# Kernel optimization log

Hardware: AMD Instinct MI355X
Metric: run time of the kernel (lower is better)

The kernel has to match this reference:

```python
import jax, jax.numpy as jnp
import numpy as np

T, B, C = 1024, 8, 256
H, F = 8, 512
D = C // H  # head dim = 32
EPS = 1e-5


def _layernorm(x, g, b):
    mu = jnp.mean(x, axis=-1, keepdims=True)
    var = jnp.var(x, axis=-1, keepdims=True)
    return (x - mu) * jax.lax.rsqrt(var + EPS) * g + b


def setup_inputs() -> dict:
    key = jax.random.key(0)
    ks = jax.random.split(key, 12)
    s = 0.02
    return {
        "x_TBC": jax.random.normal(ks[0], (T, B, C), jnp.float32),
        "key_padding_mask": jnp.zeros((B, T), dtype=bool),
        "edge_bias": jax.random.normal(ks[1], (B, H, T, T), jnp.float32),
        "ln1_g": jnp.ones((C,), jnp.float32),
        "ln1_b": jnp.zeros((C,), jnp.float32),
        "ln2_g": jnp.ones((C,), jnp.float32),
        "ln2_b": jnp.zeros((C,), jnp.float32),
        "w_qkv": jax.random.normal(ks[2], (3 * C, C), jnp.float32) * s,
        "b_qkv": jnp.zeros((3 * C,), jnp.float32),
        "w_o": jax.random.normal(ks[3], (C, C), jnp.float32) * s,
        "b_o": jnp.zeros((C,), jnp.float32),
        "w1": jax.random.normal(ks[4], (F, C), jnp.float32) * s,
        "b1": jnp.zeros((F,), jnp.float32),
        "w2": jax.random.normal(ks[5], (C, F), jnp.float32) * s,
        "b2": jnp.zeros((C,), jnp.float32),
    }


def _attn(y, key_padding_mask, edge_bias, w_qkv, b_qkv, w_o, b_o):
    # y: [T,B,C]
    qkv = jnp.einsum('tbc,ec->tbe', y, w_qkv) + b_qkv  # [T,B,3C]
    q, k, v = jnp.split(qkv, 3, axis=-1)
    def heads(z):  # [T,B,C] -> [B,H,T,D]
        return z.reshape(T, B, H, D).transpose(1, 2, 0, 3)
    q, k, v = heads(q), heads(k), heads(v)
    scale = 1.0 / jnp.sqrt(jnp.asarray(D, jnp.float32))
    scores = jnp.einsum('bhqd,bhkd->bhqk', q * scale, k) + edge_bias
    neg = jnp.asarray(-1e9, scores.dtype)
    scores = jnp.where(key_padding_mask[:, None, None, :], neg, scores)
    probs = jax.nn.softmax(scores, axis=-1)
    o = jnp.einsum('bhqk,bhkd->bhqd', probs, v)  # [B,H,T,D]
    o = o.transpose(2, 0, 1, 3).reshape(T, B, C)
    return jnp.einsum('tbc,ec->tbe', o, w_o) + b_o


def reference(x_TBC, key_padding_mask, edge_bias, ln1_g, ln1_b, ln2_g, ln2_b,
              w_qkv, b_qkv, w_o, b_o, w1, b1, w2, b2):
    # pre-LN: LN -> attn(edge bias) -> residual, LN -> FFN -> residual
    y = _layernorm(x_TBC, ln1_g, ln1_b)
    y = _attn(y, key_padding_mask, edge_bias, w_qkv, b_qkv, w_o, b_o)
    x = x_TBC + y
    y = _layernorm(x, ln2_g, ln2_b)
    y = jax.nn.gelu(jnp.einsum('tbc,fc->tbf', y, w1) + b1, approximate=False)
    y = jnp.einsum('tbf,cf->tbc', y, w2) + b2
    return x + y
```

## Files before the change

### kernel.cpp

```cpp
#include <hip/hip_runtime.h>
#include <hip/hip_bf16.h>
#include <cmath>

#define T_DIM 1024
#define B_DIM 8
#define C_DIM 256
#define H_DIM 8
#define D_DIM 32
#define F_DIM 512

typedef __attribute__((ext_vector_type(4))) float f32x4;
typedef __attribute__((ext_vector_type(8))) short bf16x8;

static __device__ __forceinline__ unsigned short f2bf(float f) {
    union { float f; unsigned u; } v; v.f = f;
    unsigned r = v.u + 0x7fff + ((v.u >> 16) & 1);
    return (unsigned short)(r >> 16);
}

__global__ __launch_bounds__(256) void convert_weights(const float* __restrict__ wqkv,
                                                       const float* __restrict__ wo,
                                                       const float* __restrict__ w1,
                                                       const float* __restrict__ w2,
                                                       unsigned short* __restrict__ dst)
{
    int e = blockIdx.x * 256 + threadIdx.x;
    const float* src; int off;
    if (e < 196608)      { src = wqkv; off = 0; }
    else if (e < 262144) { src = wo;   off = 196608; }
    else if (e < 393216) { src = w1;   off = 262144; }
    else                 { src = w2;   off = 393216; }
    dst[e] = f2bf(src[e - off]);
}

__global__ __launch_bounds__(256) void ln_bf16(const float* __restrict__ x,
                                               const float* __restrict__ g,
                                               const float* __restrict__ bta,
                                               unsigned short* __restrict__ y)
{
    int row  = blockIdx.x * 4 + (threadIdx.x >> 6);
    int lane = threadIdx.x & 63;
    float4 v = ((const float4*)(x + (size_t)row * C_DIM))[lane];
    float s  = v.x + v.y + v.z + v.w;
    float ss = v.x * v.x + v.y * v.y + v.z * v.z + v.w * v.w;
#pragma unroll
    for (int off = 1; off < 64; off <<= 1) {
        s  += __shfl_xor(s, off);
        ss += __shfl_xor(ss, off);
    }
    float mu   = s * (1.0f / C_DIM);
    float var  = ss * (1.0f / C_DIM) - mu * mu;
    float rstd = rsqrtf(var + 1e-5f);
    float4 gv = ((const float4*)g)[lane];
    float4 bv = ((const float4*)bta)[lane];
    ushort4 o;
    o.x = f2bf((v.x - mu) * rstd * gv.x + bv.x);
    o.y = f2bf((v.y - mu) * rstd * gv.y + bv.y);
    o.z = f2bf((v.z - mu) * rstd * gv.z + bv.z);
    o.w = f2bf((v.w - mu) * rstd * gv.w + bv.w);
    ((ushort4*)(y + (size_t)row * C_DIM))[lane] = o;
}

template<int EPI>
__global__ __launch_bounds__(256) void gemm_mfma(const unsigned short* __restrict__ A,
                                                 const unsigned short* __restrict__ W,
                                                 const float* __restrict__ bias,
                                                 const float* __restrict__ R,
                                                 void* __restrict__ outv,
                                                 int N, int K)
{
    __shared__ unsigned short A_s[128][40];
    __shared__ unsigned short W_s[64][40];
    int tid  = threadIdx.x;
    int lane = tid & 63;
    int wv   = tid >> 6;
    int l15  = lane & 15, lg = lane >> 4;
    int row0 = blockIdx.y * 128;
    int col0 = blockIdx.x * 64;

    f32x4 acc[2][4] = {};
    for (int k0 = 0; k0 < K; k0 += 32) {
#pragma unroll
        for (int i = 0; i < 8; i++) {
            int p = tid + i * 256;
            int m = p >> 4, dp = (p & 15) * 2;
            *(uint32_t*)&A_s[m][dp] = *(const uint32_t*)(A + (size_t)(row0 + m) * K + k0 + dp);
        }
#pragma unroll
        for (int i = 0; i < 4; i++) {
            int p = tid + i * 256;
            int n = p >> 4, dp = (p & 15) * 2;
            *(uint32_t*)&W_s[n][dp] = *(const uint32_t*)(W + (size_t)(col0 + n) * K + k0 + dp);
        }
        __syncthreads();
        bf16x8 af[2], wf[4];
#pragma unroll
        for (int mb = 0; mb < 2; mb++)
            af[mb] = *(const bf16x8*)&A_s[wv * 32 + mb * 16 + l15][lg * 8];
#pragma unroll
        for (int nb = 0; nb < 4; nb++)
            wf[nb] = *(const bf16x8*)&W_s[nb * 16 + l15][lg * 8];
#pragma unroll
        for (int mb = 0; mb < 2; mb++)
#pragma unroll
            for (int nb = 0; nb < 4; nb++)
                acc[mb][nb] = __builtin_amdgcn_mfma_f32_16x16x32_bf16(af[mb], wf[nb], acc[mb][nb], 0, 0, 0);
        __syncthreads();
    }
#pragma unroll
    for (int nb = 0; nb < 4; nb++) {
        int c = col0 + nb * 16 + l15;
        float bv = bias[c];
#pragma unroll
        for (int mb = 0; mb < 2; mb++) {
#pragma unroll
            for (int r = 0; r < 4; r++) {
                int rowm = row0 + wv * 32 + mb * 16 + lg * 4 + r;
                float v = acc[mb][nb][r] + bv;
                if (EPI == 1) v = 0.5f * v * (1.0f + erff(v * 0.70710678118654752f));
                if (EPI == 2) {
                    v += R[(size_t)rowm * N + c];
                    ((float*)outv)[(size_t)rowm * N + c] = v;
                } else {
                    ((unsigned short*)outv)[(size_t)rowm * N + c] = f2bf(v);
                }
            }
        }
    }
}

__global__ __launch_bounds__(256) void attn_mfma(const unsigned short* __restrict__ qkv,
                                                 const float* __restrict__ bias,
                                                 const unsigned char* __restrict__ mask,
                                                 unsigned short* __restrict__ o)
{
    __shared__ unsigned short K_s[64][40];
    __shared__ unsigned short Vt_s[32][72];
    __shared__ unsigned short P_s[4][16][72];
    __shared__ float bias_s[64][68];
    __shared__ unsigned char m_s[64];

    int tid  = threadIdx.x;
    int lane = tid & 63;
    int wv   = tid >> 6;
    int l15  = lane & 15, lg = lane >> 4;
    int bh = blockIdx.y, b = bh >> 3, hh = bh & 7;
    int q0 = blockIdx.x * 64;
    int qw = q0 + wv * 16;
    const float scale = 0.17677669529663687f;

    bf16x8 qf = *(const bf16x8*)(qkv + ((size_t)(qw + l15) * B_DIM + b) * 768 + hh * 32 + lg * 8);

    float m_run = -INFINITY, l_run = 0.0f;
    f32x4 oacc[2] = {};

    for (int k0 = 0; k0 < T_DIM; k0 += 64) {
#pragma unroll
        for (int i = 0; i < 4; i++) {
            int p = tid + i * 256;
            int kv = p >> 4, dp = (p & 15) * 2;
            const unsigned short* src = qkv + ((size_t)(k0 + kv) * B_DIM + b) * 768 + hh * 32;
            uint32_t kk = *(const uint32_t*)(src + 256 + dp);
            uint32_t vv = *(const uint32_t*)(src + 512 + dp);
            *(uint32_t*)&K_s[kv][dp] = kk;
            Vt_s[dp][kv]     = (unsigned short)(vv & 0xffff);
            Vt_s[dp + 1][kv] = (unsigned short)(vv >> 16);
        }
#pragma unroll
        for (int i = 0; i < 4; i++) {
            int p = tid + i * 256;
            int q = p >> 4, c4 = (p & 15) * 4;
            *(f32x4*)&bias_s[q][c4] =
                *(const f32x4*)(bias + ((size_t)bh * T_DIM + q0 + q) * T_DIM + k0 + c4);
        }
        if (tid < 64) m_s[tid] = mask[b * T_DIM + k0 + tid];
        __syncthreads();

        float sv[4][4];
        float tmax = -INFINITY;
#pragma unroll
        for (int kb = 0; kb < 4; kb++) {
            bf16x8 kf = *(const bf16x8*)&K_s[kb * 16 + l15][lg * 8];
            f32x4 z = {0.0f, 0.0f, 0.0f, 0.0f};
            f32x4 sc = __builtin_amdgcn_mfma_f32_16x16x32_bf16(kf, qf, z, 0, 0, 0);
            f32x4 bv = *(const f32x4*)&bias_s[wv * 16 + l15][kb * 16 + lg * 4];
            uint32_t mw = *(const uint32_t*)&m_s[kb * 16 + lg * 4];
#pragma unroll
            for (int r = 0; r < 4; r++) {
                float s = sc[r] * scale + bv[r];
                if ((mw >> (8 * r)) & 0xff) s = -1e9f;
                sv[kb][r] = s;
                tmax = fmaxf(tmax, s);
            }
        }
        tmax = fmaxf(tmax, __shfl_xor(tmax, 16));
        tmax = fmaxf(tmax, __shfl_xor(tmax, 32));
        float m_new = fmaxf(m_run, tmax);
        float corr = __expf(m_run - m_new);
        m_run = m_new;

        float ls = 0.0f;
#pragma unroll
        for (int kb = 0; kb < 4; kb++) {
            float p0 = __expf(sv[kb][0] - m_new);
            float p1 = __expf(sv[kb][1] - m_new);
            float p2 = __expf(sv[kb][2] - m_new);
            float p3 = __expf(sv[kb][3] - m_new);
            ls += (p0 + p1) + (p2 + p3);
            uint2 pw;
            pw.x = (uint32_t)f2bf(p0) | ((uint32_t)f2bf(p1) << 16);
            pw.y = (uint32_t)f2bf(p2) | ((uint32_t)f2bf(p3) << 16);
            *(uint2*)&P_s[wv][l15][kb * 16 + lg * 4] = pw;
        }
        ls += __shfl_xor(ls, 16);
        ls += __shfl_xor(ls, 32);
        l_run = l_run * corr + ls;
#pragma unroll
        for (int db = 0; db < 2; db++)
#pragma unroll
            for (int r = 0; r < 4; r++) oacc[db][r] *= corr;

#pragma unroll
        for (int h = 0; h < 2; h++) {
            bf16x8 pf = *(const bf16x8*)&P_s[wv][l15][h * 32 + lg * 8];
#pragma unroll
            for (int db = 0; db < 2; db++) {
                bf16x8 vf = *(const bf16x8*)&Vt_s[db * 16 + l15][h * 32 + lg * 8];
                oacc[db] = __builtin_amdgcn_mfma_f32_16x16x32_bf16(vf, pf, oacc[db], 0, 0, 0);
            }
        }
        __syncthreads();
    }

    float inv = 1.0f / l_run;
#pragma unroll
    for (int db = 0; db < 2; db++)
#pragma unroll
        for (int r = 0; r < 4; r++)
            bias_s[wv * 16 + l15][db * 16 + lg * 4 + r] = oacc[db][r] * inv;
    __syncthreads();
#pragma unroll
    for (int i = 0; i < 8; i++) {
        int p = tid + i * 256;
        int lq = p >> 5, d = p & 31;
        o[((size_t)(q0 + lq) * B_DIM + b) * C_DIM + hh * 32 + d] = f2bf(bias_s[lq][d]);
    }
}

extern "C" void kernel_launch(void* const* d_in, const int* in_sizes, int n_in,
                              void* d_out, int out_size, void* d_ws, size_t ws_size,
                              hipStream_t stream)
{
    const float* x            = (const float*)d_in[0];
    const unsigned char* mask = (const unsigned char*)d_in[1];
    const float* bias         = (const float*)d_in[2];
    const float* ln1g         = (const float*)d_in[3];
    const float* ln1b         = (const float*)d_in[4];
    const float* ln2g         = (const float*)d_in[5];
    const float* ln2b         = (const float*)d_in[6];
    const float* wqkv         = (const float*)d_in[7];
    const float* bqkv         = (const float*)d_in[8];
    const float* wo           = (const float*)d_in[9];
    const float* bo           = (const float*)d_in[10];
    const float* w1           = (const float*)d_in[11];
    const float* b1           = (const float*)d_in[12];
    const float* w2           = (const float*)d_in[13];
    const float* b2           = (const float*)d_in[14];
    float* out = (float*)d_out;
    char* ws   = (char*)d_ws;

    unsigned short* wbf     = (unsigned short*)ws;
    unsigned short* wqkv_bf = wbf;
    unsigned short* wo_bf   = wbf + 196608;
    unsigned short* w1_bf   = wbf + 262144;
    unsigned short* w2_bf   = wbf + 393216;
    unsigned short* y_bf    = (unsigned short*)(ws + (1u << 20));
    unsigned short* qkv_bf  = (unsigned short*)(ws + 5u * (1u << 20));
    unsigned short* o_bf    = (unsigned short*)(ws + 17u * (1u << 20));
    float*          x1      = (float*)(ws + 21u * (1u << 20));
    unsigned short* h_bf    = (unsigned short*)(ws + 29u * (1u << 20));

    const int M = T_DIM * B_DIM;

    convert_weights<<<2048, 256, 0, stream>>>(wqkv, wo, w1, w2, wbf);
    ln_bf16<<<M / 4, 256, 0, stream>>>(x, ln1g, ln1b, y_bf);
    gemm_mfma<0><<<dim3(768 / 64, M / 128), 256, 0, stream>>>(y_bf, wqkv_bf, bqkv, nullptr, qkv_bf, 768, 256);
    attn_mfma<<<dim3(T_DIM / 64, B_DIM * H_DIM), 256, 0, stream>>>(qkv_bf, bias, mask, o_bf);
    gemm_mfma<2><<<dim3(256 / 64, M / 128), 256, 0, stream>>>(o_bf, wo_bf, bo, x, x1, 256, 256);
    ln_bf16<<<M / 4, 256, 0, stream>>>(x1, ln2g, ln2b, y_bf);
    gemm_mfma<1><<<dim3(512 / 64, M / 128), 256, 0, stream>>>(y_bf, w1_bf, b1, nullptr, h_bf, 512, 256);
    gemm_mfma<2><<<dim3(256 / 64, M / 128), 256, 0, stream>>>(h_bf, w2_bf, b2, x1, out, 256, 512);
}
```

Measured before the change: 139.4 us.

## Use direct global-to-LDS loads with XOR swizzle and register-resident attention bias

The GEMM now stages A and W tiles with global_load_lds 16-byte transfers into XOR-swizzled shared memory and uses a larger K step of 64 per barrier. The attention kernel loads K tiles the same way, reads the edge bias straight into registers issued before the barrier instead of staging it through LDS, and writes output directly from registers. This aims to cut VGPR round-trips, bank conflicts and barrier count in the memory-bound bias stream, at the cost of relying on swizzle index math being correct and more live registers.

```diff
diff --git a/kernel.cpp b/kernel.cpp
--- a/kernel.cpp
+++ b/kernel.cpp
@@ -16,6 +16,13 @@
     union { float f; unsigned u; } v; v.f = f;
     unsigned r = v.u + 0x7fff + ((v.u >> 16) & 1);
     return (unsigned short)(r >> 16);
+}
+
+static __device__ __forceinline__ void gload_lds16(const void* g, void* l) {
+    __builtin_amdgcn_global_load_lds(
+        (const __attribute__((address_space(1))) unsigned int*)g,
+        (__attribute__((address_space(3))) unsigned int*)l,
+        16, 0, 0);
 }
 
 __global__ __launch_bounds__(256) void convert_weights(const float* __restrict__ wqkv,
@@ -69,8 +76,8 @@
                                                  void* __restrict__ outv,
                                                  int N, int K)
 {
-    __shared__ unsigned short A_s[128][40];
-    __shared__ unsigned short W_s[64][40];
+    __shared__ __align__(16) unsigned short A_s[128 * 64];
+    __shared__ __align__(16) unsigned short W_s[64 * 64];
     int tid  = threadIdx.x;
     int lane = tid & 63;
     int wv   = tid >> 6;
@@ -79,32 +86,41 @@
     int col0 = blockIdx.x * 64;
 
     f32x4 acc[2][4] = {};
-    for (int k0 = 0; k0 < K; k0 += 32) {
-#pragma unroll
-        for (int i = 0; i < 8; i++) {
-            int p = tid + i * 256;
-            int m = p >> 4, dp = (p & 15) * 2;
-            *(uint32_t*)&A_s[m][dp] = *(const uint32_t*)(A + (size_t)(row0 + m) * K + k0 + dp);
-        }
+    for (int k0 = 0; k0 < K; k0 += 64) {
 #pragma unroll
         for (int i = 0; i < 4; i++) {
-            int p = tid + i * 256;
-            int n = p >> 4, dp = (p & 15) * 2;
-            *(uint32_t*)&W_s[n][dp] = *(const uint32_t*)(W + (size_t)(col0 + n) * K + k0 + dp);
+            int u = (wv * 4 + i) * 64 + lane;
+            int r = u >> 3, c = u & 7;
+            gload_lds16(A + (size_t)(row0 + r) * K + k0 + ((c ^ (r & 7)) * 8),
+                        &A_s[(size_t)(wv * 4 + i) * 512]);
+        }
+#pragma unroll
+        for (int j = 0; j < 2; j++) {
+            int u = (wv * 2 + j) * 64 + lane;
+            int r = u >> 3, c = u & 7;
+            gload_lds16(W + (size_t)(col0 + r) * K + k0 + ((c ^ (r & 7)) * 8),
+                        &W_s[(size_t)(wv * 2 + j) * 512]);
         }
         __syncthreads();
-        bf16x8 af[2], wf[4];
-#pragma unroll
-        for (int mb = 0; mb < 2; mb++)
-            af[mb] = *(const bf16x8*)&A_s[wv * 32 + mb * 16 + l15][lg * 8];
-#pragma unroll
-        for (int nb = 0; nb < 4; nb++)
-            wf[nb] = *(const bf16x8*)&W_s[nb * 16 + l15][lg * 8];
-#pragma unroll
-        for (int mb = 0; mb < 2; mb++)
-#pragma unroll
-            for (int nb = 0; nb < 4; nb++)
-                acc[mb][nb] = __builtin_amdgcn_mfma_f32_16x16x32_bf16(af[mb], wf[nb], acc[mb][nb], 0, 0, 0);
+#pragma unroll
+        for (int kk = 0; kk < 2; kk++) {
+            bf16x8 af[2], wf[4];
+#pragma unroll
+            for (int mb = 0; mb < 2; mb++) {
+                int rowa = wv * 32 + mb * 16 + l15;
+                af[mb] = *(const bf16x8*)&A_s[rowa * 64 + (((kk * 4 + lg) ^ (l15 & 7)) * 8)];
+            }
+#pragma unroll
+            for (int nb = 0; nb < 4; nb++) {
+                int roww = nb * 16 + l15;
+                wf[nb] = *(const bf16x8*)&W_s[roww * 64 + (((kk * 4 + lg) ^ (l15 & 7)) * 8)];
+            }
+#pragma unroll
+            for (int mb = 0; mb < 2; mb++)
+#pragma unroll
+                for (int nb = 0; nb < 4; nb++)
+                    acc[mb][nb] = __builtin_amdgcn_mfma_f32_16x16x32_bf16(af[mb], wf[nb], acc[mb][nb], 0, 0, 0);
+        }
         __syncthreads();
     }
 #pragma unroll
@@ -134,10 +150,9 @@
                                                  const unsigned char* __restrict__ mask,
                                                  unsigned short* __restrict__ o)
 {
-    __shared__ unsigned short K_s[64][40];
+    __shared__ __align__(16) unsigned short K_s[64 * 32];
     __shared__ unsigned short Vt_s[32][72];
     __shared__ unsigned short P_s[4][16][72];
-    __shared__ float bias_s[64][68];
     __shared__ unsigned char m_s[64];
 
     int tid  = threadIdx.x;
@@ -151,43 +166,46 @@
 
     bf16x8 qf = *(const bf16x8*)(qkv + ((size_t)(qw + l15) * B_DIM + b) * 768 + hh * 32 + lg * 8);
 
+    int krow = wv * 16 + (lane >> 2);
+    int kc   = lane & 3;
+    int kswz = (kc ^ (krow & 3)) * 8;
+    const unsigned short* kfp = &K_s[l15 * 32 + ((lg ^ (l15 & 3)) * 8)];
+
+    const float* bptr = bias + ((size_t)bh * T_DIM + q0 + wv * 16 + l15) * T_DIM + lg * 4;
+
     float m_run = -INFINITY, l_run = 0.0f;
     f32x4 oacc[2] = {};
 
     for (int k0 = 0; k0 < T_DIM; k0 += 64) {
+        f32x4 bb0 = *(const f32x4*)(bptr + k0);
+        f32x4 bb1 = *(const f32x4*)(bptr + k0 + 16);
+        f32x4 bb2 = *(const f32x4*)(bptr + k0 + 32);
+        f32x4 bb3 = *(const f32x4*)(bptr + k0 + 48);
+        gload_lds16(qkv + ((size_t)(k0 + krow) * B_DIM + b) * 768 + 256 + hh * 32 + kswz,
+                    &K_s[(size_t)wv * 512]);
 #pragma unroll
         for (int i = 0; i < 4; i++) {
             int p = tid + i * 256;
             int kv = p >> 4, dp = (p & 15) * 2;
-            const unsigned short* src = qkv + ((size_t)(k0 + kv) * B_DIM + b) * 768 + hh * 32;
-            uint32_t kk = *(const uint32_t*)(src + 256 + dp);
-            uint32_t vv = *(const uint32_t*)(src + 512 + dp);
-            *(uint32_t*)&K_s[kv][dp] = kk;
+            uint32_t vv = *(const uint32_t*)(qkv + ((size_t)(k0 + kv) * B_DIM + b) * 768 + 512 + hh * 32 + dp);
             Vt_s[dp][kv]     = (unsigned short)(vv & 0xffff);
             Vt_s[dp + 1][kv] = (unsigned short)(vv >> 16);
         }
-#pragma unroll
-        for (int i = 0; i < 4; i++) {
-            int p = tid + i * 256;
-            int q = p >> 4, c4 = (p & 15) * 4;
-            *(f32x4*)&bias_s[q][c4] =
-                *(const f32x4*)(bias + ((size_t)bh * T_DIM + q0 + q) * T_DIM + k0 + c4);
-        }
         if (tid < 64) m_s[tid] = mask[b * T_DIM + k0 + tid];
         __syncthreads();
 
         float sv[4][4];
         float tmax = -INFINITY;
+        const f32x4 bb[4] = {bb0, bb1, bb2, bb3};
 #pragma unroll
         for (int kb = 0; kb < 4; kb++) {
-            bf16x8 kf = *(const bf16x8*)&K_s[kb * 16 + l15][lg * 8];
+            bf16x8 kf = *(const bf16x8*)(kfp + kb * 512);
             f32x4 z = {0.0f, 0.0f, 0.0f, 0.0f};
             f32x4 sc = __builtin_amdgcn_mfma_f32_16x16x32_bf16(kf, qf, z, 0, 0, 0);
-            f32x4 bv = *(const f32x4*)&bias_s[wv * 16 + l15][kb * 16 + lg * 4];
             uint32_t mw = *(const uint32_t*)&m_s[kb * 16 + lg * 4];
 #pragma unroll
             for (int r = 0; r < 4; r++) {
-                float s = sc[r] * scale + bv[r];
+                float s = sc[r] * scale + bb[kb][r];
                 if ((mw >> (8 * r)) & 0xff) s = -1e9f;
                 sv[kb][r] = s;
                 tmax = fmaxf(tmax, s);
@@ -234,16 +252,13 @@
 
     float inv = 1.0f / l_run;
 #pragma unroll
-    for (int db = 0; db < 2; db++)
-#pragma unroll
-        for (int r = 0; r < 4; r++)
-            bias_s[wv * 16 + l15][db * 16 + lg * 4 + r] = oacc[db][r] * inv;
-    __syncthreads();
-#pragma unroll
-    for (int i = 0; i < 8; i++) {
-        int p = tid + i * 256;
-        int lq = p >> 5, d = p & 31;
-        o[((size_t)(q0 + lq) * B_DIM + b) * C_DIM + hh * 32 + d] = f2bf(bias_s[lq][d]);
+    for (int db = 0; db < 2; db++) {
+        ushort4 ov;
+        ov.x = f2bf(oacc[db][0] * inv);
+        ov.y = f2bf(oacc[db][1] * inv);
+        ov.z = f2bf(oacc[db][2] * inv);
+        ov.w = f2bf(oacc[db][3] * inv);
+        *(ushort4*)(o + ((size_t)(qw + l15) * B_DIM + b) * C_DIM + hh * 32 + db * 16 + lg * 4) = ov;
     }
 }
 
```

New measurement: 138.6 us. No clear change (-0.6%).
